# Performance work log

Measured on AMD Instinct MI355X. Metric: run time of the kernel, lower is better.

The kernel has to match this reference:

```python
import jax, jax.numpy as jnp
import numpy as np

N_AZ, N_EL, N_RAD = 4, 2, 2
RADIUS = 0.05
AZ_SCALE = N_AZ / (2.0 * np.pi)
EL_SCALE = N_EL / np.pi


def setup_inputs() -> dict:
    key = jax.random.key(0)
    ks = jax.random.split(key, 7)
    B, N, M, K, C = 4, 8192, 2048, 32, 64
    return {
        "database": jax.random.normal(ks[0], (B, N, 3), dtype=jnp.float32),
        "query": jax.random.normal(ks[1], (B, M, 3), dtype=jnp.float32),
        "nn_index": jax.random.randint(ks[2], (B, M, K), 0, N, dtype=jnp.int64),
        "nn_count": jax.random.randint(ks[3], (B, M), 0, K, dtype=jnp.int32),
        "nn_dist": jax.random.uniform(ks[4], (B, M, K), dtype=jnp.float32),
        "input_features": jax.random.normal(ks[5], (B, N, C), dtype=jnp.float32),
        "filter_weights": jax.random.normal(ks[6], (N_AZ * N_EL * N_RAD, C, 1), dtype=jnp.float32),
    }


def _bins(database, query, nn_index, nn_dist):
    # Gather neighbor coordinates: (B, M, K, 3)
    neighbors = jax.vmap(lambda db, idx: db[idx])(database, nn_index)
    rel = neighbors - query[:, :, None, :]
    x, y, z = rel[..., 0], rel[..., 1], rel[..., 2]
    azimuth = jnp.arctan2(y, x) + np.pi
    elevation = jnp.arccos(jnp.clip(z / (nn_dist + 1e-8), -1.0, 1.0))
    a_bin = azimuth * AZ_SCALE
    e_bin = elevation * EL_SCALE
    r_bin = jnp.clip(nn_dist / RADIUS, 0.0, N_RAD - 1e-6)
    a_fl, e_fl, r_fl = jnp.floor(a_bin), jnp.floor(e_bin), jnp.floor(r_bin)
    a_fr, e_fr, r_fr = a_bin - a_fl, e_bin - e_fl, r_bin - r_fl
    ai, ei, ri = 1.0 - a_fr, 1.0 - e_fr, 1.0 - r_fr
    # 8 trilinear corner coefficients, torch order
    coeff = jnp.stack([
        ai * ei * ri, a_fr * ei * ri, ai * e_fr * ri, a_fr * e_fr * ri,
        ai * ei * r_fr, a_fr * ei * r_fr, ai * e_fr * r_fr, a_fr * e_fr * r_fr,
    ], axis=-1)
    a_fl = a_fl.astype(jnp.int32)
    e_fl = e_fl.astype(jnp.int32)
    r_fl = r_fl.astype(jnp.int32)
    e_c = jnp.clip(e_fl, 0, N_EL - 1)
    e_c1 = jnp.clip(e_fl + 1, 0, N_EL - 1)
    r_c = jnp.clip(r_fl, 0, N_RAD - 1)
    r_c1 = jnp.clip(r_fl + 1, 0, N_RAD - 1)
    base_a = (a_fl % N_AZ) * N_EL
    base_a1 = ((a_fl + 1) % N_AZ) * N_EL
    bin_idx = jnp.stack([
        (base_a + e_c) * N_RAD + r_c, (base_a1 + e_c) * N_RAD + r_c,
        (base_a + e_c1) * N_RAD + r_c, (base_a1 + e_c1) * N_RAD + r_c,
        (base_a + e_c) * N_RAD + r_c1, (base_a1 + e_c) * N_RAD + r_c1,
        (base_a + e_c1) * N_RAD + r_c1, (base_a1 + e_c1) * N_RAD + r_c1,
    ], axis=-1)
    return bin_idx, coeff


def reference(database, query, nn_index, nn_count, nn_dist, input_features, filter_weights):
    bin_idx, coeff = _bins(database, query, nn_index, nn_dist)  # (B,M,K,8)
    # Gather neighbor features: (B, M, K, C)
    nf = jax.vmap(lambda f, idx: f[idx])(input_features, nn_index)
    # filter_weights: (total_bins, C, 1) -> (total_bins, C); gather -> (B,M,K,8,C)
    w = filter_weights[..., 0][bin_idx]
    # Weighted sum over K neighbors and 8 interpolation corners -> (B, M, C)
    out = jnp.einsum('bmkc,bmkec,bmke->bmc', nf, w, coeff)
    return out
```

## Files before the change

### kernel.cpp

```cpp
#include <hip/hip_runtime.h>

#define B_ 4
#define N_ 8192
#define M_ 2048
#define K_ 32
#define C_ 64
#define PTS 8
#define THREADS 256

typedef float f32x2 __attribute__((ext_vector_type(2)));
typedef float f32x4 __attribute__((ext_vector_type(4)));

__device__ __forceinline__ float clampf(float x, float lo, float hi) {
    return fminf(fmaxf(x, lo), hi);
}

__global__ __launch_bounds__(THREADS) void fuzzy_kernel(
    const float* __restrict__ database,
    const float* __restrict__ query,
    const int*   __restrict__ nn_index,
    const float* __restrict__ nn_dist,
    const float* __restrict__ feats,
    const float* __restrict__ filt,
    float*       __restrict__ out)
{
    __shared__ f32x4 g[4][PTS][K_];
    __shared__ int   rowofs[PTS][K_];

    const int tid  = threadIdx.x;
    const int lane = tid & 63;

    f32x2 W2[8];
    #pragma unroll
    for (int m = 0; m < 8; ++m) {
        W2[m] = (f32x2){ filt[(2 * m) * C_ + lane], filt[(2 * m + 1) * C_ + lane] };
    }

    {
        const int pin = tid >> 5;
        const int k   = tid & 31;
        const int p   = blockIdx.x * PTS + pin;
        const int b   = p >> 11;
        const float qx = query[p * 3 + 0];
        const float qy = query[p * 3 + 1];
        const float qz = query[p * 3 + 2];
        const int   idx  = nn_index[p * K_ + k];
        const float dist = nn_dist[p * K_ + k];
        const int   bidx = b * N_ + idx;
        rowofs[pin][k] = bidx * C_;
        const float x = database[bidx * 3 + 0] - qx;
        const float y = database[bidx * 3 + 1] - qy;
        const float z = database[bidx * 3 + 2] - qz;

        const float PI_F = 3.14159265358979323846f;
        const float SC   = 0.636619772367581343f;
        float a_bin = (atan2f(y, x) + PI_F) * SC;
        float e_bin = acosf(clampf(z / (dist + 1e-8f), -1.0f, 1.0f)) * SC;
        float r_bin = clampf(dist * 20.0f, 0.0f, 1.999999f);
        float a_fl = floorf(a_bin), e_fl = floorf(e_bin), r_fl = floorf(r_bin);
        float a_fr = a_bin - a_fl, e_fr = e_bin - e_fl, r_fr = r_bin - r_fl;
        float ai = 1.0f - a_fr, ei = 1.0f - e_fr, ri = 1.0f - r_fr;
        int a_i = (int)a_fl, e_i = (int)e_fl, r_i = (int)r_fl;
        int a0 = a_i & 3, a1 = (a_i + 1) & 3;

        float E0 = (e_i < 1)  ? ei : 0.0f;
        float E1 = e_fr + ((e_i >= 1) ? ei : 0.0f);
        float R0 = (r_i == 0) ? ri : 0.0f;
        float R1 = r_fr + ((r_i == 1) ? ri : 0.0f);
        f32x4 er = (f32x4){ E0 * R0, E0 * R1, E1 * R0, E1 * R1 };
        #pragma unroll
        for (int j = 0; j < 4; ++j) {
            float Aj = (j == a0) ? ai : ((j == a1) ? a_fr : 0.0f);
            g[j][pin][k] = Aj * er;
        }
    }
    __syncthreads();

    const int wave = tid >> 6;
    const int pinA = wave * 2;
    const int pinB = pinA + 1;
    const int pA   = blockIdx.x * PTS + pinA;
    float accA = 0.0f, accB = 0.0f;

    #pragma unroll 8
    for (int k = 0; k < K_; ++k) {
        const f32x4 gA0 = g[0][pinA][k], gA1 = g[1][pinA][k];
        const f32x4 gA2 = g[2][pinA][k], gA3 = g[3][pinA][k];
        const f32x4 gB0 = g[0][pinB][k], gB1 = g[1][pinB][k];
        const f32x4 gB2 = g[2][pinB][k], gB3 = g[3][pinB][k];
        const float nfA = feats[rowofs[pinA][k] + lane];
        const float nfB = feats[rowofs[pinB][k] + lane];

        f32x2 sA = gA0.xy * W2[0] + gA0.zw * W2[1];
        sA += gA1.xy * W2[2] + gA1.zw * W2[3];
        sA += gA2.xy * W2[4] + gA2.zw * W2[5];
        sA += gA3.xy * W2[6] + gA3.zw * W2[7];
        f32x2 sB = gB0.xy * W2[0] + gB0.zw * W2[1];
        sB += gB1.xy * W2[2] + gB1.zw * W2[3];
        sB += gB2.xy * W2[4] + gB2.zw * W2[5];
        sB += gB3.xy * W2[6] + gB3.zw * W2[7];

        accA += nfA * (sA.x + sA.y);
        accB += nfB * (sB.x + sB.y);
    }
    out[pA * C_ + lane]       = accA;
    out[(pA + 1) * C_ + lane] = accB;
}

extern "C" void kernel_launch(void* const* d_in, const int* in_sizes, int n_in,
                              void* d_out, int out_size, void* d_ws, size_t ws_size,
                              hipStream_t stream) {
    const float* database = (const float*)d_in[0];
    const float* query    = (const float*)d_in[1];
    const int*   nn_index = (const int*)d_in[2];
    const float* nn_dist  = (const float*)d_in[4];
    const float* feats    = (const float*)d_in[5];
    const float* filt     = (const float*)d_in[6];
    float* out = (float*)d_out;

    dim3 grid((B_ * M_) / PTS);
    dim3 block(THREADS);
    hipLaunchKernelGGL(fuzzy_kernel, grid, block, 0, stream,
                       database, query, nn_index, nn_dist, feats, filt, out);
}
```

Before: 89.72 us.

## Pack interpolation coefficients and filter weights as fp16, use fdot2 accumulation

Stores the 16 per-neighbor bin coefficients as packed fp16 in shared memory, halving LDS footprint and read traffic, and converts the filter weights to fp16 pairs. The inner loop uses v_dot2 fp16 dot products with fp32 accumulation in place of packed fp32 FMAs. Row offsets are now read directly from nn_index through a wave-uniform base rather than from an LDS table, and the wave index is made scalar with readfirstlane. This reduces ALU and LDS work but rounds weights and coefficients to fp16, which may cost accuracy.

```diff
diff --git a/kernel.cpp b/kernel.cpp
--- a/kernel.cpp
+++ b/kernel.cpp
@@ -8,8 +8,22 @@
 #define PTS 8
 #define THREADS 256
 
-typedef float f32x2 __attribute__((ext_vector_type(2)));
-typedef float f32x4 __attribute__((ext_vector_type(4)));
+typedef float     f32x4 __attribute__((ext_vector_type(4)));
+typedef _Float16  h2    __attribute__((ext_vector_type(2)));
+typedef _Float16  h8    __attribute__((ext_vector_type(8)));
+
+__device__ __forceinline__ h2 pkrtz(float a, float b) {
+    return __builtin_bit_cast(h2, __builtin_amdgcn_cvt_pkrtz(a, b));
+}
+
+#if defined(__has_builtin)
+#if __has_builtin(__builtin_amdgcn_fdot2)
+#define FDOT2(a, b, c) __builtin_amdgcn_fdot2((a), (b), (c), false)
+#endif
+#endif
+#ifndef FDOT2
+#define FDOT2(a, b, c) ((float)(a)[0] * (float)(b)[0] + (float)(a)[1] * (float)(b)[1] + (c))
+#endif
 
 __device__ __forceinline__ float clampf(float x, float lo, float hi) {
     return fminf(fmaxf(x, lo), hi);
@@ -24,16 +38,15 @@
     const float* __restrict__ filt,
     float*       __restrict__ out)
 {
-    __shared__ f32x4 g[4][PTS][K_];
-    __shared__ int   rowofs[PTS][K_];
+    __shared__ h8 g[PTS * K_][2];
 
     const int tid  = threadIdx.x;
     const int lane = tid & 63;
 
-    f32x2 W2[8];
+    h2 Wh[8];
     #pragma unroll
     for (int m = 0; m < 8; ++m) {
-        W2[m] = (f32x2){ filt[(2 * m) * C_ + lane], filt[(2 * m + 1) * C_ + lane] };
+        Wh[m] = pkrtz(filt[(2 * m) * C_ + lane], filt[(2 * m + 1) * C_ + lane]);
     }
 
     {
@@ -47,7 +60,6 @@
         const int   idx  = nn_index[p * K_ + k];
         const float dist = nn_dist[p * K_ + k];
         const int   bidx = b * N_ + idx;
-        rowofs[pin][k] = bidx * C_;
         const float x = database[bidx * 3 + 0] - qx;
         const float y = database[bidx * 3 + 1] - qy;
         const float z = database[bidx * 3 + 2] - qz;
@@ -68,40 +80,65 @@
         float R0 = (r_i == 0) ? ri : 0.0f;
         float R1 = r_fr + ((r_i == 1) ? ri : 0.0f);
         f32x4 er = (f32x4){ E0 * R0, E0 * R1, E1 * R0, E1 * R1 };
+
+        float A[4];
         #pragma unroll
-        for (int j = 0; j < 4; ++j) {
-            float Aj = (j == a0) ? ai : ((j == a1) ? a_fr : 0.0f);
-            g[j][pin][k] = Aj * er;
-        }
+        for (int j = 0; j < 4; ++j)
+            A[j] = (j == a0) ? ai : ((j == a1) ? a_fr : 0.0f);
+
+        h2 q00 = pkrtz(A[0] * er.x, A[0] * er.y);
+        h2 q01 = pkrtz(A[0] * er.z, A[0] * er.w);
+        h2 q10 = pkrtz(A[1] * er.x, A[1] * er.y);
+        h2 q11 = pkrtz(A[1] * er.z, A[1] * er.w);
+        h2 q20 = pkrtz(A[2] * er.x, A[2] * er.y);
+        h2 q21 = pkrtz(A[2] * er.z, A[2] * er.w);
+        h2 q30 = pkrtz(A[3] * er.x, A[3] * er.y);
+        h2 q31 = pkrtz(A[3] * er.z, A[3] * er.w);
+
+        h8 lo = (h8){ q00[0], q00[1], q01[0], q01[1], q10[0], q10[1], q11[0], q11[1] };
+        h8 hi = (h8){ q20[0], q20[1], q21[0], q21[1], q30[0], q30[1], q31[0], q31[1] };
+        g[tid][0] = lo;
+        g[tid][1] = hi;
     }
     __syncthreads();
 
-    const int wave = tid >> 6;
+    const int wave = __builtin_amdgcn_readfirstlane(tid >> 6);
     const int pinA = wave * 2;
     const int pinB = pinA + 1;
     const int pA   = blockIdx.x * PTS + pinA;
+    const int b    = pA >> 11;
+
+    const int* __restrict__ nnA = nn_index + pA * K_;
+    const int* __restrict__ nnB = nnA + K_;
+    const float* __restrict__ fb = feats + (size_t)b * (N_ * C_) + lane;
+
     float accA = 0.0f, accB = 0.0f;
 
     #pragma unroll 8
     for (int k = 0; k < K_; ++k) {
-        const f32x4 gA0 = g[0][pinA][k], gA1 = g[1][pinA][k];
-        const f32x4 gA2 = g[2][pinA][k], gA3 = g[3][pinA][k];
-        const f32x4 gB0 = g[0][pinB][k], gB1 = g[1][pinB][k];
-        const f32x4 gB2 = g[2][pinB][k], gB3 = g[3][pinB][k];
-        const float nfA = feats[rowofs[pinA][k] + lane];
-        const float nfB = feats[rowofs[pinB][k] + lane];
+        const int rA = nnA[k];
+        const int rB = nnB[k];
+        const h8 gA0 = g[pinA * K_ + k][0];
+        const h8 gA1 = g[pinA * K_ + k][1];
+        const h8 gB0 = g[pinB * K_ + k][0];
+        const h8 gB1 = g[pinB * K_ + k][1];
+        const float nfA = fb[(size_t)rA << 6];
+        const float nfB = fb[(size_t)rB << 6];
 
-        f32x2 sA = gA0.xy * W2[0] + gA0.zw * W2[1];
-        sA += gA1.xy * W2[2] + gA1.zw * W2[3];
-        sA += gA2.xy * W2[4] + gA2.zw * W2[5];
-        sA += gA3.xy * W2[6] + gA3.zw * W2[7];
-        f32x2 sB = gB0.xy * W2[0] + gB0.zw * W2[1];
-        sB += gB1.xy * W2[2] + gB1.zw * W2[3];
-        sB += gB2.xy * W2[4] + gB2.zw * W2[5];
-        sB += gB3.xy * W2[6] + gB3.zw * W2[7];
-
-        accA += nfA * (sA.x + sA.y);
-        accB += nfB * (sB.x + sB.y);
+        float sA = 0.0f, sB = 0.0f;
+        #pragma unroll
+        for (int m = 0; m < 4; ++m) {
+            h2 a0p = (h2){ gA0[2 * m], gA0[2 * m + 1] };
+            h2 a1p = (h2){ gA1[2 * m], gA1[2 * m + 1] };
+            h2 b0p = (h2){ gB0[2 * m], gB0[2 * m + 1] };
+            h2 b1p = (h2){ gB1[2 * m], gB1[2 * m + 1] };
+            sA = FDOT2(a0p, Wh[m], sA);
+            sA = FDOT2(a1p, Wh[m + 4], sA);
+            sB = FDOT2(b0p, Wh[m], sB);
+            sB = FDOT2(b1p, Wh[m + 4], sB);
+        }
+        accA += nfA * sA;
+        accB += nfB * sB;
     }
     out[pA * C_ + lane]       = accA;
     out[(pA + 1) * C_ + lane] = accB;
```

Result: faster. 84.11 us (-6.3%).
